# Kernel optimization log

Measured on AMD Instinct MI355X. Metric: run time of the kernel, lower is better.

Reference implementation:

```python
import jax, jax.numpy as jnp
import numpy as np

NEG_SLOPE = 0.2   # PyG GATConv leaky_relu default
BN_EPS = 1e-5


def setup_inputs() -> dict:
    key = jax.random.key(0)
    ks = jax.random.split(key, 6)
    B, C, N, T = 8, 128, 64, 512   # batch, in_channels, electrodes, time_steps
    H, D = 4, 32                   # heads, per-head dim; OUT = H*D = 128
    E = 256                        # knn edges (k=4 per electrode)
    OUT = H * D
    x = jax.random.normal(ks[0], (B, C, N, T), dtype=jnp.float32)
    W = jax.random.normal(ks[1], (C, H, D), dtype=jnp.float32) / np.float32(np.sqrt(C))
    att_src = jax.random.normal(ks[2], (H, D), dtype=jnp.float32) / np.float32(np.sqrt(D))
    att_dst = jax.random.normal(ks[3], (H, D), dtype=jnp.float32) / np.float32(np.sqrt(D))
    bias = jnp.zeros((OUT,), dtype=jnp.float32)
    bn_gamma = jnp.ones((OUT,), jnp.float32)
    bn_beta = jnp.zeros((OUT,), jnp.float32)
    bn_mean = jnp.zeros((OUT,), jnp.float32)   # BatchNorm running stats (eval mode)
    bn_var = jnp.ones((OUT,), jnp.float32)
    edge_index = jax.random.randint(ks[4], (2, E), 0, N, dtype=jnp.int32)
    return dict(x=x, W=W, att_src=att_src, att_dst=att_dst, bias=bias,
                bn_gamma=bn_gamma, bn_beta=bn_beta, bn_mean=bn_mean,
                bn_var=bn_var, edge_index=edge_index)


def _gat(x, W, att_src, att_dst, bias, edge_index):
    # x: [BT, N, C]; fixed graph shared across all BT slices -> fully batched
    BT, N, C = x.shape
    H, D = att_src.shape
    loops = jnp.arange(N, dtype=edge_index.dtype)
    src = jnp.concatenate([edge_index[0], loops])   # GATConv add_self_loops=True
    dst = jnp.concatenate([edge_index[1], loops])   # [E']
    h = jnp.einsum('bnc,chd->bnhd', x, W)           # [BT,N,H,D]
    a_src = jnp.einsum('bnhd,hd->bnh', h, att_src)  # [BT,N,H]
    a_dst = jnp.einsum('bnhd,hd->bnh', h, att_dst)
    scores = jax.nn.leaky_relu(a_src[:, src] + a_dst[:, dst], NEG_SLOPE)  # [BT,E',H]
    scores_e = jnp.transpose(scores, (1, 0, 2))                           # [E',BT,H]
    # segment softmax over incoming edges of each target node
    m = jax.ops.segment_max(scores_e, dst, num_segments=N)               # [N,BT,H]
    ex = jnp.exp(scores_e - m[dst])
    denom = jax.ops.segment_sum(ex, dst, num_segments=N)
    alpha = ex / denom[dst]                                               # [E',BT,H]
    msgs = alpha[..., None] * jnp.transpose(h[:, src], (1, 0, 2, 3))      # [E',BT,H,D]
    agg = jax.ops.segment_sum(msgs, dst, num_segments=N)                  # [N,BT,H,D]
    out = jnp.transpose(agg, (1, 0, 2, 3)).reshape(BT, N, H * D) + bias   # concat heads
    return out


def reference(x, W, att_src, att_dst, bias, bn_gamma, bn_beta, bn_mean, bn_var, edge_index):
    B, C, N, T = x.shape
    xt = jnp.transpose(x, (0, 3, 2, 1)).reshape(B * T, N, C)  # loop dim batched
    g = _gat(xt, W, att_src, att_dst, bias, edge_index)        # [BT,N,OUT]
    g = g.mean(axis=1)                                         # mean over nodes -> [BT,OUT]
    OUT = g.shape[-1]
    g = g.reshape(B, T, OUT).transpose(0, 2, 1)                # [B,OUT,T]
    y = (g - bn_mean[:, None]) * jax.lax.rsqrt(bn_var[:, None] + BN_EPS) \
        * bn_gamma[:, None] + bn_beta[:, None]                 # BatchNorm1d (eval)
    return y[:, :, None, :]                                    # [B,OUT,1,T]
```

## Files before the change

### kernel.cpp

```cpp
#include <hip/hip_runtime.h>
#include <math.h>

#define B_ 8
#define C_ 128
#define N_ 64
#define T_ 512
#define H_ 4
#define D_ 32
#define OUT_ 128
#define E_ 256
#define EP_ 320
#define NEG_SLOPE 0.2f
#define BN_EPS 1e-5f
#define TC 8

__global__ void setup_kernel(const float* __restrict__ W,
                             const float* __restrict__ att_src,
                             const float* __restrict__ att_dst,
                             const int* __restrict__ edge_index,
                             float* __restrict__ wa,
                             int* __restrict__ iOff_g, int* __restrict__ iSrc_g,
                             int* __restrict__ oOff_g, int* __restrict__ oDst_g) {
  __shared__ int icnt[N_], ibase[N_ + 1], ifill[N_];
  __shared__ int ocnt[N_], obase[N_ + 1], ofill[N_];
  __shared__ int esrc[EP_], edst[EP_];
  int tid = threadIdx.x;

  for (int idx = tid; idx < C_ * 8; idx += blockDim.x) {
    int c = idx >> 3, j = idx & 7, h = j & 3;
    const float* att = (j < 4) ? att_src : att_dst;
    float s = 0.f;
    for (int d = 0; d < D_; ++d)
      s += W[(c * H_ + h) * D_ + d] * att[h * D_ + d];
    wa[idx] = s;
  }
  if (tid < N_) { icnt[tid] = 0; ifill[tid] = 0; ocnt[tid] = 0; ofill[tid] = 0; }
  __syncthreads();
  for (int e = tid; e < EP_; e += blockDim.x) {
    int s, d;
    if (e < E_) { s = edge_index[e]; d = edge_index[E_ + e]; }
    else        { s = e - E_;        d = e - E_; }
    esrc[e] = s; edst[e] = d;
    atomicAdd(&icnt[d], 1);
    atomicAdd(&ocnt[s], 1);
  }
  __syncthreads();
  if (tid == 0) {
    int ai = 0, ao = 0;
    for (int n = 0; n < N_; ++n) {
      ibase[n] = ai; ai += icnt[n];
      obase[n] = ao; ao += ocnt[n];
    }
    ibase[N_] = ai; obase[N_] = ao;
  }
  __syncthreads();
  if (tid <= N_) { iOff_g[tid] = ibase[tid]; oOff_g[tid] = obase[tid]; }
  for (int e = tid; e < EP_; e += blockDim.x) {
    int s = esrc[e], d = edst[e];
    int pi = ibase[d] + atomicAdd(&ifill[d], 1);
    iSrc_g[pi] = s;
    int po = obase[s] + atomicAdd(&ofill[s], 1);
    oDst_g[po] = d;
  }
}

__global__ __launch_bounds__(256, 2)
void mega_kernel(const float* __restrict__ x,
                 const float* __restrict__ wa_g,
                 const float* __restrict__ W,
                 const int* __restrict__ iOff_g, const int* __restrict__ iSrc_g,
                 const int* __restrict__ oOff_g, const int* __restrict__ oDst_g,
                 const float* __restrict__ bias,
                 const float* __restrict__ bn_gamma,
                 const float* __restrict__ bn_beta,
                 const float* __restrict__ bn_mean,
                 const float* __restrict__ bn_var,
                 float* __restrict__ out) {
  __shared__ float a_l[8 * 64 * 12];
  __shared__ float m_l[64 * 9 * 4];
  __shared__ float inv_l[64 * 9 * 4];
  __shared__ float w_l[64 * 36];
  __shared__ float wal[C_ * 8];
  __shared__ int iOff[N_ + 1], oOff[N_ + 1];
  __shared__ int iSrc[EP_], oDst[EP_];

  const int tid = threadIdx.x;
  const int b = blockIdx.x & 7;
  const int tchunk = blockIdx.x >> 3;
  const int t0 = tchunk * TC;

  for (int i = tid; i < EP_; i += 256) { iSrc[i] = iSrc_g[i]; oDst[i] = oDst_g[i]; }
  if (tid <= N_) { iOff[tid] = iOff_g[tid]; oOff[tid] = oOff_g[tid]; }
  for (int i = tid; i < C_ * 8; i += 256) wal[i] = wa_g[i];
  __syncthreads();

  {
    const int n1 = tid >> 2, q = tid & 3;
    const float* xp = x + ((size_t)(b * C_) * N_ + n1) * T_ + t0 + q * 2;
    float acc[8][2];
#pragma unroll
    for (int j = 0; j < 8; ++j) { acc[j][0] = 0.f; acc[j][1] = 0.f; }
#pragma unroll 8
    for (int c = 0; c < C_; ++c) {
      float2 xv = *reinterpret_cast<const float2*>(xp + (size_t)c * (N_ * T_));
#pragma unroll
      for (int j = 0; j < 8; ++j) {
        float wj = wal[c * 8 + j];
        acc[j][0] = fmaf(xv.x, wj, acc[j][0]);
        acc[j][1] = fmaf(xv.y, wj, acc[j][1]);
      }
    }
#pragma unroll
    for (int j = 0; j < 8; ++j) {
      float2 v; v.x = acc[j][0]; v.y = acc[j][1];
      *reinterpret_cast<float2*>(&a_l[j * 768 + n1 * 12 + q * 2]) = v;
    }
  }
  __syncthreads();

  {
    const int t = tid & 7, grp = tid >> 3;
#pragma unroll
    for (int rep = 0; rep < 2; ++rep) {
      int nd = grp + rep * 32;
      int e0 = iOff[nd], e1 = iOff[nd + 1];
      float ad0 = a_l[4 * 768 + nd * 12 + t];
      float ad1 = a_l[5 * 768 + nd * 12 + t];
      float ad2 = a_l[6 * 768 + nd * 12 + t];
      float ad3 = a_l[7 * 768 + nd * 12 + t];
      float m0 = -1e30f, m1 = -1e30f, m2 = -1e30f, m3 = -1e30f;
      for (int e = e0; e < e1; ++e) {
        int s = iSrc[e];
        float v0 = a_l[0 * 768 + s * 12 + t] + ad0; v0 = v0 > 0.f ? v0 : NEG_SLOPE * v0;
        float v1 = a_l[1 * 768 + s * 12 + t] + ad1; v1 = v1 > 0.f ? v1 : NEG_SLOPE * v1;
        float v2 = a_l[2 * 768 + s * 12 + t] + ad2; v2 = v2 > 0.f ? v2 : NEG_SLOPE * v2;
        float v3 = a_l[3 * 768 + s * 12 + t] + ad3; v3 = v3 > 0.f ? v3 : NEG_SLOPE * v3;
        m0 = fmaxf(m0, v0); m1 = fmaxf(m1, v1);
        m2 = fmaxf(m2, v2); m3 = fmaxf(m3, v3);
      }
      float d0 = 0.f, d1 = 0.f, d2 = 0.f, d3 = 0.f;
      for (int e = e0; e < e1; ++e) {
        int s = iSrc[e];
        float v0 = a_l[0 * 768 + s * 12 + t] + ad0; v0 = v0 > 0.f ? v0 : NEG_SLOPE * v0;
        float v1 = a_l[1 * 768 + s * 12 + t] + ad1; v1 = v1 > 0.f ? v1 : NEG_SLOPE * v1;
        float v2 = a_l[2 * 768 + s * 12 + t] + ad2; v2 = v2 > 0.f ? v2 : NEG_SLOPE * v2;
        float v3 = a_l[3 * 768 + s * 12 + t] + ad3; v3 = v3 > 0.f ? v3 : NEG_SLOPE * v3;
        d0 += __expf(v0 - m0); d1 += __expf(v1 - m1);
        d2 += __expf(v2 - m2); d3 += __expf(v3 - m3);
      }
      float4 mv; mv.x = m0; mv.y = m1; mv.z = m2; mv.w = m3;
      float4 iv; iv.x = 1.f / (d0 * (float)N_); iv.y = 1.f / (d1 * (float)N_);
      iv.z = 1.f / (d2 * (float)N_); iv.w = 1.f / (d3 * (float)N_);
      *reinterpret_cast<float4*>(&m_l[(nd * 9 + t) * 4]) = mv;
      *reinterpret_cast<float4*>(&inv_l[(nd * 9 + t) * 4]) = iv;
    }
  }
  __syncthreads();

  {
    const int t = tid & 7, grp = tid >> 3;
#pragma unroll
    for (int rep = 0; rep < 2; ++rep) {
      int src = grp + rep * 32;
      int e0 = oOff[src], e1 = oOff[src + 1];
      float as0 = a_l[0 * 768 + src * 12 + t];
      float as1 = a_l[1 * 768 + src * 12 + t];
      float as2 = a_l[2 * 768 + src * 12 + t];
      float as3 = a_l[3 * 768 + src * 12 + t];
      float w0 = 0.f, w1 = 0.f, w2 = 0.f, w3 = 0.f;
      for (int e = e0; e < e1; ++e) {
        int d = oDst[e];
        float4 mv = *reinterpret_cast<const float4*>(&m_l[(d * 9 + t) * 4]);
        float4 iv = *reinterpret_cast<const float4*>(&inv_l[(d * 9 + t) * 4]);
        float v0 = as0 + a_l[4 * 768 + d * 12 + t]; v0 = v0 > 0.f ? v0 : NEG_SLOPE * v0;
        float v1 = as1 + a_l[5 * 768 + d * 12 + t]; v1 = v1 > 0.f ? v1 : NEG_SLOPE * v1;
        float v2 = as2 + a_l[6 * 768 + d * 12 + t]; v2 = v2 > 0.f ? v2 : NEG_SLOPE * v2;
        float v3 = as3 + a_l[7 * 768 + d * 12 + t]; v3 = v3 > 0.f ? v3 : NEG_SLOPE * v3;
        w0 += __expf(v0 - mv.x) * iv.x;
        w1 += __expf(v1 - mv.y) * iv.y;
        w2 += __expf(v2 - mv.z) * iv.z;
        w3 += __expf(v3 - mv.w) * iv.w;
      }
      w_l[src * 36 +  0 + t] = w0;
      w_l[src * 36 +  8 + t] = w1;
      w_l[src * 36 + 16 + t] = w2;
      w_l[src * 36 + 24 + t] = w3;
    }
  }
  __syncthreads();

  {
    const int cl = tid >> 1, g = tid & 1;
    const float* xb = x + ((size_t)(b * C_) + cl) * N_ * T_ + t0 + g * 4;
    float yr[4][4];
#pragma unroll
    for (int h = 0; h < 4; ++h)
#pragma unroll
      for (int tt = 0; tt < 4; ++tt) yr[h][tt] = 0.f;
#pragma unroll 8
    for (int n = 0; n < N_; ++n) {
      float4 xv = *reinterpret_cast<const float4*>(xb + (size_t)n * T_);
#pragma unroll
      for (int h = 0; h < 4; ++h) {
        float4 wv = *reinterpret_cast<const float4*>(&w_l[n * 36 + h * 8 + g * 4]);
        yr[h][0] = fmaf(xv.x, wv.x, yr[h][0]);
        yr[h][1] = fmaf(xv.y, wv.y, yr[h][1]);
        yr[h][2] = fmaf(xv.z, wv.z, yr[h][2]);
        yr[h][3] = fmaf(xv.w, wv.w, yr[h][3]);
      }
    }
    float* y_l = a_l;
#pragma unroll
    for (int h = 0; h < 4; ++h) {
      float4 v; v.x = yr[h][0]; v.y = yr[h][1]; v.z = yr[h][2]; v.w = yr[h][3];
      y_l[h * 1152 + cl * 9 + g * 4 + 0] = v.x;
      y_l[h * 1152 + cl * 9 + g * 4 + 1] = v.y;
      y_l[h * 1152 + cl * 9 + g * 4 + 2] = v.z;
      y_l[h * 1152 + cl * 9 + g * 4 + 3] = v.w;
    }
  }
  __syncthreads();

  {
    const int t3 = tid & 7, g3 = tid >> 3;
    const int h = g3 >> 3, d0 = (g3 & 7) * 4;
    const float* y_l = a_l;
    float acc[4] = {0.f, 0.f, 0.f, 0.f};
#pragma unroll 4
    for (int c = 0; c < C_; ++c) {
      float yv = y_l[h * 1152 + c * 9 + t3];
      const float4 wv = *reinterpret_cast<const float4*>(
          &W[((size_t)c * H_ + h) * D_ + d0]);
      acc[0] = fmaf(yv, wv.x, acc[0]); acc[1] = fmaf(yv, wv.y, acc[1]);
      acc[2] = fmaf(yv, wv.z, acc[2]); acc[3] = fmaf(yv, wv.w, acc[3]);
    }
#pragma unroll
    for (int k = 0; k < 4; ++k) {
      int oc = h * D_ + d0 + k;
      float scale = bn_gamma[oc] * rsqrtf(bn_var[oc] + BN_EPS);
      float shift = bn_beta[oc] - bn_mean[oc] * scale;
      out[((size_t)b * OUT_ + oc) * T_ + t0 + t3] =
          (acc[k] + bias[oc]) * scale + shift;
    }
  }
}

extern "C" void kernel_launch(void* const* d_in, const int* in_sizes, int n_in,
                              void* d_out, int out_size, void* d_ws, size_t ws_size,
                              hipStream_t stream) {
  const float* x        = (const float*)d_in[0];
  const float* W        = (const float*)d_in[1];
  const float* att_src  = (const float*)d_in[2];
  const float* att_dst  = (const float*)d_in[3];
  const float* bias     = (const float*)d_in[4];
  const float* bn_gamma = (const float*)d_in[5];
  const float* bn_beta  = (const float*)d_in[6];
  const float* bn_mean  = (const float*)d_in[7];
  const float* bn_var   = (const float*)d_in[8];
  const int* edge_index = (const int*)d_in[9];
  float* out = (float*)d_out;

  char* ws = (char*)d_ws;
  float* wa   = (float*)ws;
  int* iOff_g = (int*)(ws + 4096);
  int* iSrc_g = (int*)(ws + 4608);
  int* oOff_g = (int*)(ws + 6144);
  int* oDst_g = (int*)(ws + 6656);

  setup_kernel<<<1, 256, 0, stream>>>(W, att_src, att_dst, edge_index, wa,
                                      iOff_g, iSrc_g, oOff_g, oDst_g);
  mega_kernel<<<512, 256, 0, stream>>>(x, wa, W, iOff_g, iSrc_g, oOff_g, oDst_g,
                                       bias, bn_gamma, bn_beta, bn_mean, bn_var,
                                       out);
}
```

Baseline: 81.77 us.

## Split channel reduction across thread halves with float4 batched loads and folded softmax scale

The first projection phase now gives each thread float4 time slices and splits the channel loop between two halves of the block, which are combined through a shared-memory reduction. Eight global loads are issued before the FMAs in both x-reading phases, aiming to raise memory-level parallelism and hide latency. The softmax max and inverse-denominator are merged into one factor exp(-m)/denom, which removes a shared load and a subtraction per edge. Computing exp(v) without subtracting the max can overflow for large scores, and the extra shared buffer plus the added barrier raise LDS use.

```diff
diff --git a/kernel.cpp b/kernel.cpp
--- a/kernel.cpp
+++ b/kernel.cpp
@@ -63,6 +63,12 @@
     oDst_g[po] = d;
   }
 }
+
+#define P1FMA(J, WS) \
+  acc[J].x = fmaf(xv[u].x, WS, acc[J].x); \
+  acc[J].y = fmaf(xv[u].y, WS, acc[J].y); \
+  acc[J].z = fmaf(xv[u].z, WS, acc[J].z); \
+  acc[J].w = fmaf(xv[u].w, WS, acc[J].w);
 
 __global__ __launch_bounds__(256, 2)
 void mega_kernel(const float* __restrict__ x,
@@ -77,8 +83,8 @@
                  const float* __restrict__ bn_var,
                  float* __restrict__ out) {
   __shared__ float a_l[8 * 64 * 12];
-  __shared__ float m_l[64 * 9 * 4];
-  __shared__ float inv_l[64 * 9 * 4];
+  __shared__ float4 red4[8 * 128];
+  __shared__ float z_l[64 * 9 * 4];
   __shared__ float w_l[64 * 36];
   __shared__ float wal[C_ * 8];
   __shared__ int iOff[N_ + 1], oOff[N_ + 1];
@@ -95,28 +101,43 @@
   __syncthreads();
 
   {
-    const int n1 = tid >> 2, q = tid & 3;
-    const float* xp = x + ((size_t)(b * C_) * N_ + n1) * T_ + t0 + q * 2;
-    float acc[8][2];
-#pragma unroll
-    for (int j = 0; j < 8; ++j) { acc[j][0] = 0.f; acc[j][1] = 0.f; }
-#pragma unroll 8
-    for (int c = 0; c < C_; ++c) {
-      float2 xv = *reinterpret_cast<const float2*>(xp + (size_t)c * (N_ * T_));
+    const int cpar = __builtin_amdgcn_readfirstlane(tid >> 7);
+    const int r = tid & 127;
+    const int n1 = r >> 1, th = r & 1;
+    const float* xp = x + ((size_t)(b * C_ + cpar) * N_ + n1) * T_ + t0 + th * 4;
+    float4 acc[8];
+#pragma unroll
+    for (int j = 0; j < 8; ++j) { acc[j].x = 0.f; acc[j].y = 0.f; acc[j].z = 0.f; acc[j].w = 0.f; }
+    for (int kb = 0; kb < 8; ++kb) {
+      float4 xv[8];
+#pragma unroll
+      for (int u = 0; u < 8; ++u)
+        xv[u] = *reinterpret_cast<const float4*>(xp + (size_t)(kb * 16 + u * 2) * (N_ * T_));
+#pragma unroll
+      for (int u = 0; u < 8; ++u) {
+        const int c = cpar + (kb * 8 + u) * 2;
+        const float4 w0 = *reinterpret_cast<const float4*>(&wal[c * 8]);
+        const float4 w1 = *reinterpret_cast<const float4*>(&wal[c * 8 + 4]);
+        P1FMA(0, w0.x) P1FMA(1, w0.y) P1FMA(2, w0.z) P1FMA(3, w0.w)
+        P1FMA(4, w1.x) P1FMA(5, w1.y) P1FMA(6, w1.z) P1FMA(7, w1.w)
+      }
+    }
+    if (cpar == 1) {
+#pragma unroll
+      for (int j = 0; j < 8; ++j) red4[j * 128 + r] = acc[j];
+    }
+    __syncthreads();
+    if (cpar == 0) {
 #pragma unroll
       for (int j = 0; j < 8; ++j) {
-        float wj = wal[c * 8 + j];
-        acc[j][0] = fmaf(xv.x, wj, acc[j][0]);
-        acc[j][1] = fmaf(xv.y, wj, acc[j][1]);
-      }
-    }
-#pragma unroll
-    for (int j = 0; j < 8; ++j) {
-      float2 v; v.x = acc[j][0]; v.y = acc[j][1];
-      *reinterpret_cast<float2*>(&a_l[j * 768 + n1 * 12 + q * 2]) = v;
-    }
-  }
-  __syncthreads();
+        float4 o = red4[j * 128 + r];
+        float* ap = &a_l[j * 768 + n1 * 12 + th * 4];
+        ap[0] = acc[j].x + o.x; ap[1] = acc[j].y + o.y;
+        ap[2] = acc[j].z + o.z; ap[3] = acc[j].w + o.w;
+      }
+    }
+    __syncthreads();
+  }
 
   {
     const int t = tid & 7, grp = tid >> 3;
@@ -148,11 +169,12 @@
         d0 += __expf(v0 - m0); d1 += __expf(v1 - m1);
         d2 += __expf(v2 - m2); d3 += __expf(v3 - m3);
       }
-      float4 mv; mv.x = m0; mv.y = m1; mv.z = m2; mv.w = m3;
-      float4 iv; iv.x = 1.f / (d0 * (float)N_); iv.y = 1.f / (d1 * (float)N_);
-      iv.z = 1.f / (d2 * (float)N_); iv.w = 1.f / (d3 * (float)N_);
-      *reinterpret_cast<float4*>(&m_l[(nd * 9 + t) * 4]) = mv;
-      *reinterpret_cast<float4*>(&inv_l[(nd * 9 + t) * 4]) = iv;
+      float4 zv;
+      zv.x = __expf(-m0) / (d0 * (float)N_);
+      zv.y = __expf(-m1) / (d1 * (float)N_);
+      zv.z = __expf(-m2) / (d2 * (float)N_);
+      zv.w = __expf(-m3) / (d3 * (float)N_);
+      *reinterpret_cast<float4*>(&z_l[(nd * 9 + t) * 4]) = zv;
     }
   }
   __syncthreads();
@@ -170,16 +192,15 @@
       float w0 = 0.f, w1 = 0.f, w2 = 0.f, w3 = 0.f;
       for (int e = e0; e < e1; ++e) {
         int d = oDst[e];
-        float4 mv = *reinterpret_cast<const float4*>(&m_l[(d * 9 + t) * 4]);
-        float4 iv = *reinterpret_cast<const float4*>(&inv_l[(d * 9 + t) * 4]);
+        float4 zv = *reinterpret_cast<const float4*>(&z_l[(d * 9 + t) * 4]);
         float v0 = as0 + a_l[4 * 768 + d * 12 + t]; v0 = v0 > 0.f ? v0 : NEG_SLOPE * v0;
         float v1 = as1 + a_l[5 * 768 + d * 12 + t]; v1 = v1 > 0.f ? v1 : NEG_SLOPE * v1;
         float v2 = as2 + a_l[6 * 768 + d * 12 + t]; v2 = v2 > 0.f ? v2 : NEG_SLOPE * v2;
         float v3 = as3 + a_l[7 * 768 + d * 12 + t]; v3 = v3 > 0.f ? v3 : NEG_SLOPE * v3;
-        w0 += __expf(v0 - mv.x) * iv.x;
-        w1 += __expf(v1 - mv.y) * iv.y;
-        w2 += __expf(v2 - mv.z) * iv.z;
-        w3 += __expf(v3 - mv.w) * iv.w;
+        w0 += __expf(v0) * zv.x;
+        w1 += __expf(v1) * zv.y;
+        w2 += __expf(v2) * zv.z;
+        w3 += __expf(v3) * zv.w;
       }
       w_l[src * 36 +  0 + t] = w0;
       w_l[src * 36 +  8 + t] = w1;
@@ -192,31 +213,34 @@
   {
     const int cl = tid >> 1, g = tid & 1;
     const float* xb = x + ((size_t)(b * C_) + cl) * N_ * T_ + t0 + g * 4;
-    float yr[4][4];
-#pragma unroll
-    for (int h = 0; h < 4; ++h)
-#pragma unroll
-      for (int tt = 0; tt < 4; ++tt) yr[h][tt] = 0.f;
-#pragma unroll 8
-    for (int n = 0; n < N_; ++n) {
-      float4 xv = *reinterpret_cast<const float4*>(xb + (size_t)n * T_);
-#pragma unroll
-      for (int h = 0; h < 4; ++h) {
-        float4 wv = *reinterpret_cast<const float4*>(&w_l[n * 36 + h * 8 + g * 4]);
-        yr[h][0] = fmaf(xv.x, wv.x, yr[h][0]);
-        yr[h][1] = fmaf(xv.y, wv.y, yr[h][1]);
-        yr[h][2] = fmaf(xv.z, wv.z, yr[h][2]);
-        yr[h][3] = fmaf(xv.w, wv.w, yr[h][3]);
+    float4 yr[4];
+#pragma unroll
+    for (int h = 0; h < 4; ++h) { yr[h].x = 0.f; yr[h].y = 0.f; yr[h].z = 0.f; yr[h].w = 0.f; }
+    for (int nb = 0; nb < 8; ++nb) {
+      float4 xv[8];
+#pragma unroll
+      for (int u = 0; u < 8; ++u)
+        xv[u] = *reinterpret_cast<const float4*>(xb + (size_t)(nb * 8 + u) * T_);
+#pragma unroll
+      for (int u = 0; u < 8; ++u) {
+        const int n = nb * 8 + u;
+#pragma unroll
+        for (int h = 0; h < 4; ++h) {
+          float4 wv = *reinterpret_cast<const float4*>(&w_l[n * 36 + h * 8 + g * 4]);
+          yr[h].x = fmaf(xv[u].x, wv.x, yr[h].x);
+          yr[h].y = fmaf(xv[u].y, wv.y, yr[h].y);
+          yr[h].z = fmaf(xv[u].z, wv.z, yr[h].z);
+          yr[h].w = fmaf(xv[u].w, wv.w, yr[h].w);
+        }
       }
     }
     float* y_l = a_l;
 #pragma unroll
     for (int h = 0; h < 4; ++h) {
-      float4 v; v.x = yr[h][0]; v.y = yr[h][1]; v.z = yr[h][2]; v.w = yr[h][3];
-      y_l[h * 1152 + cl * 9 + g * 4 + 0] = v.x;
-      y_l[h * 1152 + cl * 9 + g * 4 + 1] = v.y;
-      y_l[h * 1152 + cl * 9 + g * 4 + 2] = v.z;
-      y_l[h * 1152 + cl * 9 + g * 4 + 3] = v.w;
+      y_l[h * 1152 + cl * 9 + g * 4 + 0] = yr[h].x;
+      y_l[h * 1152 + cl * 9 + g * 4 + 1] = yr[h].y;
+      y_l[h * 1152 + cl * 9 + g * 4 + 2] = yr[h].z;
+      y_l[h * 1152 + cl * 9 + g * 4 + 3] = yr[h].w;
     }
   }
   __syncthreads();
```

After: 82.49 us. No clear change (+0.9%).

## Pre-transpose x into bf16 tiles and fuse GAT into a 512-thread kernel

Applied to the files above, without the earlier changes.

Adds a transpose kernel that converts x to bf16 and lays it out as contiguous per-(batch, time-chunk) tiles. The fused kernel then loads each tile once into swizzled LDS and reuses it for both the attention-logit pass and the aggregation pass, instead of reading x from global memory twice with strided access. The outgoing-edge CSR pass is replaced by LDS atomic scatter of the attention weights. The cost is an extra kernel and a full read plus write of x, and the bf16 rounding of x lowers accuracy.

```diff
diff --git a/kernel.cpp b/kernel.cpp
--- a/kernel.cpp
+++ b/kernel.cpp
@@ -12,17 +12,23 @@
 #define EP_ 320
 #define NEG_SLOPE 0.2f
 #define BN_EPS 1e-5f
-#define TC 8
+
+__device__ inline unsigned short f2bf(float f) {
+  unsigned u = __float_as_uint(f);
+  u += 0x7FFFu + ((u >> 16) & 1u);
+  return (unsigned short)(u >> 16);
+}
+__device__ inline float bf2f(unsigned short s) {
+  return __uint_as_float(((unsigned)s) << 16);
+}
 
 __global__ void setup_kernel(const float* __restrict__ W,
                              const float* __restrict__ att_src,
                              const float* __restrict__ att_dst,
                              const int* __restrict__ edge_index,
                              float* __restrict__ wa,
-                             int* __restrict__ iOff_g, int* __restrict__ iSrc_g,
-                             int* __restrict__ oOff_g, int* __restrict__ oDst_g) {
+                             int* __restrict__ iOff_g, int* __restrict__ iSrc_g) {
   __shared__ int icnt[N_], ibase[N_ + 1], ifill[N_];
-  __shared__ int ocnt[N_], obase[N_ + 1], ofill[N_];
   __shared__ int esrc[EP_], edst[EP_];
   int tid = threadIdx.x;
 
@@ -34,7 +40,7 @@
       s += W[(c * H_ + h) * D_ + d] * att[h * D_ + d];
     wa[idx] = s;
   }
-  if (tid < N_) { icnt[tid] = 0; ifill[tid] = 0; ocnt[tid] = 0; ofill[tid] = 0; }
+  if (tid < N_) { icnt[tid] = 0; ifill[tid] = 0; }
   __syncthreads();
   for (int e = tid; e < EP_; e += blockDim.x) {
     int s, d;
@@ -42,206 +48,207 @@
     else        { s = e - E_;        d = e - E_; }
     esrc[e] = s; edst[e] = d;
     atomicAdd(&icnt[d], 1);
-    atomicAdd(&ocnt[s], 1);
   }
   __syncthreads();
   if (tid == 0) {
-    int ai = 0, ao = 0;
-    for (int n = 0; n < N_; ++n) {
-      ibase[n] = ai; ai += icnt[n];
-      obase[n] = ao; ao += ocnt[n];
-    }
-    ibase[N_] = ai; obase[N_] = ao;
-  }
-  __syncthreads();
-  if (tid <= N_) { iOff_g[tid] = ibase[tid]; oOff_g[tid] = obase[tid]; }
+    int ai = 0;
+    for (int n = 0; n < N_; ++n) { ibase[n] = ai; ai += icnt[n]; }
+    ibase[N_] = ai;
+  }
+  __syncthreads();
+  if (tid <= N_) iOff_g[tid] = ibase[tid];
   for (int e = tid; e < EP_; e += blockDim.x) {
-    int s = esrc[e], d = edst[e];
+    int d = edst[e];
     int pi = ibase[d] + atomicAdd(&ifill[d], 1);
-    iSrc_g[pi] = s;
-    int po = obase[s] + atomicAdd(&ofill[s], 1);
-    oDst_g[po] = d;
-  }
-}
-
-__global__ __launch_bounds__(256, 2)
-void mega_kernel(const float* __restrict__ x,
-                 const float* __restrict__ wa_g,
-                 const float* __restrict__ W,
-                 const int* __restrict__ iOff_g, const int* __restrict__ iSrc_g,
-                 const int* __restrict__ oOff_g, const int* __restrict__ oDst_g,
-                 const float* __restrict__ bias,
-                 const float* __restrict__ bn_gamma,
-                 const float* __restrict__ bn_beta,
-                 const float* __restrict__ bn_mean,
-                 const float* __restrict__ bn_var,
-                 float* __restrict__ out) {
-  __shared__ float a_l[8 * 64 * 12];
-  __shared__ float m_l[64 * 9 * 4];
-  __shared__ float inv_l[64 * 9 * 4];
-  __shared__ float w_l[64 * 36];
-  __shared__ float wal[C_ * 8];
-  __shared__ int iOff[N_ + 1], oOff[N_ + 1];
-  __shared__ int iSrc[EP_], oDst[EP_];
-
+    iSrc_g[pi] = esrc[e];
+  }
+}
+
+__global__ __launch_bounds__(512, 2)
+void trans_kernel(const float* __restrict__ x,
+                  unsigned short* __restrict__ xs) {
+  __shared__ unsigned short tile[N_ * 520];
   const int tid = threadIdx.x;
   const int b = blockIdx.x & 7;
-  const int tchunk = blockIdx.x >> 3;
-  const int t0 = tchunk * TC;
-
-  for (int i = tid; i < EP_; i += 256) { iSrc[i] = iSrc_g[i]; oDst[i] = oDst_g[i]; }
-  if (tid <= N_) { iOff[tid] = iOff_g[tid]; oOff[tid] = oOff_g[tid]; }
-  for (int i = tid; i < C_ * 8; i += 256) wal[i] = wa_g[i];
-  __syncthreads();
-
-  {
-    const int n1 = tid >> 2, q = tid & 3;
-    const float* xp = x + ((size_t)(b * C_) * N_ + n1) * T_ + t0 + q * 2;
-    float acc[8][2];
-#pragma unroll
-    for (int j = 0; j < 8; ++j) { acc[j][0] = 0.f; acc[j][1] = 0.f; }
-#pragma unroll 8
+  const int c = blockIdx.x >> 3;
+
+  const float4* xp = reinterpret_cast<const float4*>(
+      x + ((size_t)(b * C_ + c)) * (N_ * T_));
+#pragma unroll
+  for (int k = 0; k < 16; ++k) {
+    int g = tid + k * 512;
+    float4 v = xp[g];
+    int n = g >> 7;
+    int tcol = (g & 127) * 4;
+    ushort4 s;
+    s.x = f2bf(v.x); s.y = f2bf(v.y); s.z = f2bf(v.z); s.w = f2bf(v.w);
+    *reinterpret_cast<ushort4*>(&tile[n * 520 + tcol]) = s;
+  }
+  __syncthreads();
+
+  const int tcl = tid >> 6;
+  const int n   = tid & 63;
+#pragma unroll
+  for (int p = 0; p < 8; ++p) {
+    const int tc = p * 8 + tcl;
+    uint4 v = *reinterpret_cast<const uint4*>(&tile[n * 520 + tc * 8]);
+    unsigned short* dst = xs +
+        ((((size_t)(b * 64 + tc) * C_ + c) * N_) + n) * 8;
+    *reinterpret_cast<uint4*>(dst) = v;
+  }
+}
+
+__global__ __launch_bounds__(512, 1)
+void fused_kernel(const unsigned short* __restrict__ xs,
+                  const float* __restrict__ wa_g,
+                  const float* __restrict__ Wm,
+                  const int* __restrict__ iOff_g, const int* __restrict__ iSrc_g,
+                  const float* __restrict__ bias,
+                  const float* __restrict__ bn_gamma,
+                  const float* __restrict__ bn_beta,
+                  const float* __restrict__ bn_mean,
+                  const float* __restrict__ bn_var,
+                  float* __restrict__ out) {
+  __shared__ unsigned short xt[C_ * 512];
+  __shared__ float a_l[8 * N_ * 8];
+  __shared__ float w_l[N_ * 4 * 8];
+  __shared__ float wal[C_ * 8];
+  __shared__ int iSrc[EP_];
+  __shared__ int iOff[N_ + 1];
+
+  const int tid = threadIdx.x;
+  const int b  = blockIdx.x & 7;
+  const int tc = blockIdx.x >> 3;
+  const int t0 = tc * 8;
+
+  for (int i = tid; i < C_ * 8; i += 512) wal[i] = wa_g[i];
+  if (tid < EP_) iSrc[tid] = iSrc_g[tid];
+  if (tid >= EP_ && tid < EP_ + N_ + 1) iOff[tid - EP_] = iOff_g[tid - EP_];
+  for (int i = tid; i < N_ * 4 * 8; i += 512) w_l[i] = 0.f;
+
+  {
+    const uint4* src = reinterpret_cast<const uint4*>(
+        xs + ((size_t)(b * 64 + tc) * C_) * 512);
+#pragma unroll
+    for (int k = 0; k < 16; ++k) {
+      int g = tid + k * 512;
+      uint4 v = src[g];
+      int c = g >> 6;
+      int u = g & 63;
+      int dstb = c * 1024 + ((u * 16) ^ ((c & 7) << 4));
+      *reinterpret_cast<uint4*>(reinterpret_cast<char*>(xt) + dstb) = v;
+    }
+  }
+  __syncthreads();
+
+  const int n_  = tid >> 3;
+  const int t_  = tid & 7;
+
+  {
+    float av[8] = {0.f,0.f,0.f,0.f,0.f,0.f,0.f,0.f};
     for (int c = 0; c < C_; ++c) {
-      float2 xv = *reinterpret_cast<const float2*>(xp + (size_t)c * (N_ * T_));
-#pragma unroll
-      for (int j = 0; j < 8; ++j) {
-        float wj = wal[c * 8 + j];
-        acc[j][0] = fmaf(xv.x, wj, acc[j][0]);
-        acc[j][1] = fmaf(xv.y, wj, acc[j][1]);
+      float xv = bf2f(xt[c * 512 + ((n_ ^ (c & 7)) * 8 + t_)]);
+      const float4 w0 = *reinterpret_cast<const float4*>(&wal[c * 8]);
+      const float4 w1 = *reinterpret_cast<const float4*>(&wal[c * 8 + 4]);
+      av[0] = fmaf(xv, w0.x, av[0]); av[1] = fmaf(xv, w0.y, av[1]);
+      av[2] = fmaf(xv, w0.z, av[2]); av[3] = fmaf(xv, w0.w, av[3]);
+      av[4] = fmaf(xv, w1.x, av[4]); av[5] = fmaf(xv, w1.y, av[5]);
+      av[6] = fmaf(xv, w1.z, av[6]); av[7] = fmaf(xv, w1.w, av[7]);
+    }
+#pragma unroll
+    for (int j = 0; j < 8; ++j) a_l[j * 512 + n_ * 8 + t_] = av[j];
+  }
+  __syncthreads();
+
+  {
+    int e0 = iOff[n_], e1 = iOff[n_ + 1];
+    float ad0 = a_l[4 * 512 + n_ * 8 + t_];
+    float ad1 = a_l[5 * 512 + n_ * 8 + t_];
+    float ad2 = a_l[6 * 512 + n_ * 8 + t_];
+    float ad3 = a_l[7 * 512 + n_ * 8 + t_];
+    float m0 = -1e30f, m1 = -1e30f, m2 = -1e30f, m3 = -1e30f;
+    for (int e = e0; e < e1; ++e) {
+      int s = iSrc[e];
+      float v0 = a_l[0 * 512 + s * 8 + t_] + ad0; v0 = v0 > 0.f ? v0 : NEG_SLOPE * v0;
+      float v1 = a_l[1 * 512 + s * 8 + t_] + ad1; v1 = v1 > 0.f ? v1 : NEG_SLOPE * v1;
+      float v2 = a_l[2 * 512 + s * 8 + t_] + ad2; v2 = v2 > 0.f ? v2 : NEG_SLOPE * v2;
+      float v3 = a_l[3 * 512 + s * 8 + t_] + ad3; v3 = v3 > 0.f ? v3 : NEG_SLOPE * v3;
+      m0 = fmaxf(m0, v0); m1 = fmaxf(m1, v1);
+      m2 = fmaxf(m2, v2); m3 = fmaxf(m3, v3);
+    }
+    float d0 = 0.f, d1 = 0.f, d2 = 0.f, d3 = 0.f;
+    for (int e = e0; e < e1; ++e) {
+      int s = iSrc[e];
+      float v0 = a_l[0 * 512 + s * 8 + t_] + ad0; v0 = v0 > 0.f ? v0 : NEG_SLOPE * v0;
+      float v1 = a_l[1 * 512 + s * 8 + t_] + ad1; v1 = v1 > 0.f ? v1 : NEG_SLOPE * v1;
+      float v2 = a_l[2 * 512 + s * 8 + t_] + ad2; v2 = v2 > 0.f ? v2 : NEG_SLOPE * v2;
+      float v3 = a_l[3 * 512 + s * 8 + t_] + ad3; v3 = v3 > 0.f ? v3 : NEG_SLOPE * v3;
+      d0 += __expf(v0 - m0); d1 += __expf(v1 - m1);
+      d2 += __expf(v2 - m2); d3 += __expf(v3 - m3);
+    }
+    float i0 = 1.f / (d0 * (float)N_);
+    float i1 = 1.f / (d1 * (float)N_);
+    float i2 = 1.f / (d2 * (float)N_);
+    float i3 = 1.f / (d3 * (float)N_);
+    for (int e = e0; e < e1; ++e) {
+      int s = iSrc[e];
+      float v0 = a_l[0 * 512 + s * 8 + t_] + ad0; v0 = v0 > 0.f ? v0 : NEG_SLOPE * v0;
+      float v1 = a_l[1 * 512 + s * 8 + t_] + ad1; v1 = v1 > 0.f ? v1 : NEG_SLOPE * v1;
+      float v2 = a_l[2 * 512 + s * 8 + t_] + ad2; v2 = v2 > 0.f ? v2 : NEG_SLOPE * v2;
+      float v3 = a_l[3 * 512 + s * 8 + t_] + ad3; v3 = v3 > 0.f ? v3 : NEG_SLOPE * v3;
+      atomicAdd(&w_l[(s * 4 + 0) * 8 + t_], __expf(v0 - m0) * i0);
+      atomicAdd(&w_l[(s * 4 + 1) * 8 + t_], __expf(v1 - m1) * i1);
+      atomicAdd(&w_l[(s * 4 + 2) * 8 + t_], __expf(v2 - m2) * i2);
+      atomicAdd(&w_l[(s * 4 + 3) * 8 + t_], __expf(v3 - m3) * i3);
+    }
+  }
+  __syncthreads();
+
+  {
+    const int c  = tid >> 2;
+    const int tp = tid & 3;
+    float y0[4] = {0.f,0.f,0.f,0.f};
+    float y1[4] = {0.f,0.f,0.f,0.f};
+    for (int n = 0; n < N_; ++n) {
+      ushort2 xv = *reinterpret_cast<const ushort2*>(
+          &xt[c * 512 + ((n ^ (c & 7)) * 8 + tp * 2)]);
+      float x0 = bf2f(xv.x), x1 = bf2f(xv.y);
+#pragma unroll
+      for (int h = 0; h < 4; ++h) {
+        float2 wv = *reinterpret_cast<const float2*>(&w_l[(n * 4 + h) * 8 + tp * 2]);
+        y0[h] = fmaf(x0, wv.x, y0[h]);
+        y1[h] = fmaf(x1, wv.y, y1[h]);
       }
     }
-#pragma unroll
-    for (int j = 0; j < 8; ++j) {
-      float2 v; v.x = acc[j][0]; v.y = acc[j][1];
-      *reinterpret_cast<float2*>(&a_l[j * 768 + n1 * 12 + q * 2]) = v;
-    }
-  }
-  __syncthreads();
-
-  {
-    const int t = tid & 7, grp = tid >> 3;
-#pragma unroll
-    for (int rep = 0; rep < 2; ++rep) {
-      int nd = grp + rep * 32;
-      int e0 = iOff[nd], e1 = iOff[nd + 1];
-      float ad0 = a_l[4 * 768 + nd * 12 + t];
-      float ad1 = a_l[5 * 768 + nd * 12 + t];
-      float ad2 = a_l[6 * 768 + nd * 12 + t];
-      float ad3 = a_l[7 * 768 + nd * 12 + t];
-      float m0 = -1e30f, m1 = -1e30f, m2 = -1e30f, m3 = -1e30f;
-      for (int e = e0; e < e1; ++e) {
-        int s = iSrc[e];
-        float v0 = a_l[0 * 768 + s * 12 + t] + ad0; v0 = v0 > 0.f ? v0 : NEG_SLOPE * v0;
-        float v1 = a_l[1 * 768 + s * 12 + t] + ad1; v1 = v1 > 0.f ? v1 : NEG_SLOPE * v1;
-        float v2 = a_l[2 * 768 + s * 12 + t] + ad2; v2 = v2 > 0.f ? v2 : NEG_SLOPE * v2;
-        float v3 = a_l[3 * 768 + s * 12 + t] + ad3; v3 = v3 > 0.f ? v3 : NEG_SLOPE * v3;
-        m0 = fmaxf(m0, v0); m1 = fmaxf(m1, v1);
-        m2 = fmaxf(m2, v2); m3 = fmaxf(m3, v3);
-      }
-      float d0 = 0.f, d1 = 0.f, d2 = 0.f, d3 = 0.f;
-      for (int e = e0; e < e1; ++e) {
-        int s = iSrc[e];
-        float v0 = a_l[0 * 768 + s * 12 + t] + ad0; v0 = v0 > 0.f ? v0 : NEG_SLOPE * v0;
-        float v1 = a_l[1 * 768 + s * 12 + t] + ad1; v1 = v1 > 0.f ? v1 : NEG_SLOPE * v1;
-        float v2 = a_l[2 * 768 + s * 12 + t] + ad2; v2 = v2 > 0.f ? v2 : NEG_SLOPE * v2;
-        float v3 = a_l[3 * 768 + s * 12 + t] + ad3; v3 = v3 > 0.f ? v3 : NEG_SLOPE * v3;
-        d0 += __expf(v0 - m0); d1 += __expf(v1 - m1);
-        d2 += __expf(v2 - m2); d3 += __expf(v3 - m3);
-      }
-      float4 mv; mv.x = m0; mv.y = m1; mv.z = m2; mv.w = m3;
-      float4 iv; iv.x = 1.f / (d0 * (float)N_); iv.y = 1.f / (d1 * (float)N_);
-      iv.z = 1.f / (d2 * (float)N_); iv.w = 1.f / (d3 * (float)N_);
-      *reinterpret_cast<float4*>(&m_l[(nd * 9 + t) * 4]) = mv;
-      *reinterpret_cast<float4*>(&inv_l[(nd * 9 + t) * 4]) = iv;
-    }
-  }
-  __syncthreads();
-
-  {
-    const int t = tid & 7, grp = tid >> 3;
-#pragma unroll
-    for (int rep = 0; rep < 2; ++rep) {
-      int src = grp + rep * 32;
-      int e0 = oOff[src], e1 = oOff[src + 1];
-      float as0 = a_l[0 * 768 + src * 12 + t];
-      float as1 = a_l[1 * 768 + src * 12 + t];
-      float as2 = a_l[2 * 768 + src * 12 + t];
-      float as3 = a_l[3 * 768 + src * 12 + t];
-      float w0 = 0.f, w1 = 0.f, w2 = 0.f, w3 = 0.f;
-      for (int e = e0; e < e1; ++e) {
-        int d = oDst[e];
-        float4 mv = *reinterpret_cast<const float4*>(&m_l[(d * 9 + t) * 4]);
-        float4 iv = *reinterpret_cast<const float4*>(&inv_l[(d * 9 + t) * 4]);
-        float v0 = as0 + a_l[4 * 768 + d * 12 + t]; v0 = v0 > 0.f ? v0 : NEG_SLOPE * v0;
-        float v1 = as1 + a_l[5 * 768 + d * 12 + t]; v1 = v1 > 0.f ? v1 : NEG_SLOPE * v1;
-        float v2 = as2 + a_l[6 * 768 + d * 12 + t]; v2 = v2 > 0.f ? v2 : NEG_SLOPE * v2;
-        float v3 = as3 + a_l[7 * 768 + d * 12 + t]; v3 = v3 > 0.f ? v3 : NEG_SLOPE * v3;
-        w0 += __expf(v0 - mv.x) * iv.x;
-        w1 += __expf(v1 - mv.y) * iv.y;
-        w2 += __expf(v2 - mv.z) * iv.z;
-        w3 += __expf(v3 - mv.w) * iv.w;
-      }
-      w_l[src * 36 +  0 + t] = w0;
-      w_l[src * 36 +  8 + t] = w1;
-      w_l[src * 36 + 16 + t] = w2;
-      w_l[src * 36 + 24 + t] = w3;
-    }
-  }
-  __syncthreads();
-
-  {
-    const int cl = tid >> 1, g = tid & 1;
-    const float* xb = x + ((size_t)(b * C_) + cl) * N_ * T_ + t0 + g * 4;
-    float yr[4][4];
-#pragma unroll
-    for (int h = 0; h < 4; ++h)
-#pragma unroll
-      for (int tt = 0; tt < 4; ++tt) yr[h][tt] = 0.f;
-#pragma unroll 8
-    for (int n = 0; n < N_; ++n) {
-      float4 xv = *reinterpret_cast<const float4*>(xb + (size_t)n * T_);
-#pragma unroll
-      for (int h = 0; h < 4; ++h) {
-        float4 wv = *reinterpret_cast<const float4*>(&w_l[n * 36 + h * 8 + g * 4]);
-        yr[h][0] = fmaf(xv.x, wv.x, yr[h][0]);
-        yr[h][1] = fmaf(xv.y, wv.y, yr[h][1]);
-        yr[h][2] = fmaf(xv.z, wv.z, yr[h][2]);
-        yr[h][3] = fmaf(xv.w, wv.w, yr[h][3]);
-      }
-    }
-    float* y_l = a_l;
+    __syncthreads();
 #pragma unroll
     for (int h = 0; h < 4; ++h) {
-      float4 v; v.x = yr[h][0]; v.y = yr[h][1]; v.z = yr[h][2]; v.w = yr[h][3];
-      y_l[h * 1152 + cl * 9 + g * 4 + 0] = v.x;
-      y_l[h * 1152 + cl * 9 + g * 4 + 1] = v.y;
-      y_l[h * 1152 + cl * 9 + g * 4 + 2] = v.z;
-      y_l[h * 1152 + cl * 9 + g * 4 + 3] = v.w;
-    }
-  }
-  __syncthreads();
-
-  {
-    const int t3 = tid & 7, g3 = tid >> 3;
-    const int h = g3 >> 3, d0 = (g3 & 7) * 4;
-    const float* y_l = a_l;
-    float acc[4] = {0.f, 0.f, 0.f, 0.f};
+      a_l[(h * C_ + c) * 8 + tp * 2]     = y0[h];
+      a_l[(h * C_ + c) * 8 + tp * 2 + 1] = y1[h];
+    }
+  }
+  __syncthreads();
+
+  {
+    const int h  = tid >> 7;
+    const int r  = (tid >> 3) & 15;
+    const int te = tid & 7;
+    float o0 = 0.f, o1 = 0.f;
 #pragma unroll 4
     for (int c = 0; c < C_; ++c) {
-      float yv = y_l[h * 1152 + c * 9 + t3];
-      const float4 wv = *reinterpret_cast<const float4*>(
-          &W[((size_t)c * H_ + h) * D_ + d0]);
-      acc[0] = fmaf(yv, wv.x, acc[0]); acc[1] = fmaf(yv, wv.y, acc[1]);
-      acc[2] = fmaf(yv, wv.z, acc[2]); acc[3] = fmaf(yv, wv.w, acc[3]);
-    }
-#pragma unroll
-    for (int k = 0; k < 4; ++k) {
-      int oc = h * D_ + d0 + k;
-      float scale = bn_gamma[oc] * rsqrtf(bn_var[oc] + BN_EPS);
-      float shift = bn_beta[oc] - bn_mean[oc] * scale;
-      out[((size_t)b * OUT_ + oc) * T_ + t0 + t3] =
-          (acc[k] + bias[oc]) * scale + shift;
-    }
+      float yv = a_l[(h * C_ + c) * 8 + te];
+      const float2 wv = *reinterpret_cast<const float2*>(
+          &Wm[((size_t)c * H_ + h) * D_ + r * 2]);
+      o0 = fmaf(yv, wv.x, o0);
+      o1 = fmaf(yv, wv.y, o1);
+    }
+    int oc = h * D_ + r * 2;
+    float s0 = bn_gamma[oc] * rsqrtf(bn_var[oc] + BN_EPS);
+    float s1 = bn_gamma[oc + 1] * rsqrtf(bn_var[oc + 1] + BN_EPS);
+    out[((size_t)b * OUT_ + oc) * T_ + t0 + te] =
+        (o0 + bias[oc]) * s0 + bn_beta[oc] - bn_mean[oc] * s0;
+    out[((size_t)b * OUT_ + oc + 1) * T_ + t0 + te] =
+        (o1 + bias[oc + 1]) * s1 + bn_beta[oc + 1] - bn_mean[oc + 1] * s1;
   }
 }
 
@@ -264,12 +271,12 @@
   float* wa   = (float*)ws;
   int* iOff_g = (int*)(ws + 4096);
   int* iSrc_g = (int*)(ws + 4608);
-  int* oOff_g = (int*)(ws + 6144);
-  int* oDst_g = (int*)(ws + 6656);
-
-  setup_kernel<<<1, 256, 0, stream>>>(W, att_src, att_dst, edge_index, wa,
-                                      iOff_g, iSrc_g, oOff_g, oDst_g);
-  mega_kernel<<<512, 256, 0, stream>>>(x, wa, W, iOff_g, iSrc_g, oOff_g, oDst_g,
-                                       bias, bn_gamma, bn_beta, bn_mean, bn_var,
-                                       out);
-}
+  unsigned short* xs = (unsigned short*)(ws + 16384);
+
+  setup_kernel<<<1, 256, 0, stream>>>(W, att_src, att_dst, edge_index,
+                                      wa, iOff_g, iSrc_g);
+  trans_kernel<<<1024, 512, 0, stream>>>(x, xs);
+  fused_kernel<<<512, 512, 0, stream>>>(xs, wa, W, iOff_g, iSrc_g,
+                                        bias, bn_gamma, bn_beta, bn_mean, bn_var,
+                                        out);
+}
```

After: 125.6 us. 53.6% more time.
